# Optimization experiments

Measured on AMD Instinct MI355X. Metric: run time of the kernel, lower is better.

Reference implementation:

```python
import jax, jax.numpy as jnp
import numpy as np

N = 30000      # nodes
E = 480000     # edges
F = 128        # num_node_features (== C, required by LSTM-JK stacking of h_list incl. x)
C = 128        # graph_hidden_channels
K = 8          # kernel_size (num gaussians)
D = 2          # pseudo-coordinate dim
L = 4          # nlayers
H = (L * C) // 2   # PyG JK-LSTM hidden size = 256
NHID = 512
NOUT = 256
B = 1024       # number of graphs in batch
EPS = 1e-15


def setup_inputs() -> dict:
    key = jax.random.key(0)
    ks = jax.random.split(key, 24)
    s = 0.05
    inp = {}
    inp['x'] = jax.random.normal(ks[0], (N, F), jnp.float32)
    inp['edge_index'] = jax.random.randint(ks[1], (2, E), 0, N, dtype=jnp.int32)
    inp['edge_attr'] = jax.random.uniform(ks[2], (E, D), jnp.float32)
    inp['batch'] = jnp.sort(jax.random.randint(ks[3], (N,), 0, B, dtype=jnp.int32))
    # GMMConv params per layer (Cin == C for all layers since F == C)
    inp['g'] = jax.random.normal(ks[4], (L, F, K * C), jnp.float32) * s
    inp['root'] = jax.random.normal(ks[5], (L, F, C), jnp.float32) * s
    inp['bias'] = jnp.zeros((L, C), jnp.float32)
    inp['mu'] = jax.random.uniform(ks[6], (L, K, D), jnp.float32)
    inp['sigma'] = jax.random.uniform(ks[7], (L, K, D), jnp.float32) * 0.5 + 0.5
    inp['bn_gamma'] = jnp.ones((L, C), jnp.float32)
    inp['bn_beta'] = jnp.zeros((L, C), jnp.float32)
    # Bidirectional LSTM for JumpingKnowledge: dir 0 = fwd, dir 1 = bwd; gate order i,f,g,o
    inp['w_ih'] = jax.random.normal(ks[8], (2, 4 * H, C), jnp.float32) * s
    inp['w_hh'] = jax.random.normal(ks[9], (2, 4 * H, H), jnp.float32) * s
    inp['b_ih'] = jnp.zeros((2, 4 * H), jnp.float32)
    inp['b_hh'] = jnp.zeros((2, 4 * H), jnp.float32)
    inp['att_w'] = jax.random.normal(ks[10], (2 * H, 1), jnp.float32) * s
    inp['att_b'] = jnp.zeros((1,), jnp.float32)
    inp['p1_w'] = jax.random.normal(ks[11], (C, NHID), jnp.float32) * s
    inp['p1_b'] = jnp.zeros((NHID,), jnp.float32)
    inp['p2_w'] = jax.random.normal(ks[12], (NHID, NOUT), jnp.float32) * s
    inp['p2_b'] = jnp.zeros((NOUT,), jnp.float32)
    inp['ln_g'] = jnp.ones((NOUT,), jnp.float32)
    inp['ln_b'] = jnp.zeros((NOUT,), jnp.float32)
    return inp


def _lstm_dir(xs, w_ih, w_hh, b_ih, b_hh, reverse):
    # xs: [T, N, C] -> hidden states [T, N, H], aligned with input order
    def step(carry, xt):
        h, c = carry
        gates = xt @ w_ih.T + h @ w_hh.T + (b_ih + b_hh)
        i, f, g, o = jnp.split(gates, 4, axis=-1)
        c = jax.nn.sigmoid(f) * c + jax.nn.sigmoid(i) * jnp.tanh(g)
        h = jax.nn.sigmoid(o) * jnp.tanh(c)
        return (h, c), h
    h0 = jnp.zeros((xs.shape[1], w_hh.shape[1]), xs.dtype)
    _, hs = jax.lax.scan(step, (h0, h0), xs, reverse=reverse)
    return hs


def reference(x, edge_index, edge_attr, batch, g, root, bias, mu, sigma,
              bn_gamma, bn_beta, w_ih, w_hh, b_ih, b_hh, att_w, att_b,
              p1_w, p1_b, p2_w, p2_b, ln_g, ln_b):
    src, dst = edge_index[0], edge_index[1]
    deg = jnp.maximum(jax.ops.segment_sum(jnp.ones((E,), x.dtype), dst, num_segments=N), 1.0)[:, None]
    h = x
    h_list = [x]
    for i in range(L):
        # GMMConv: node-level transform then gaussian-weighted message passing (mean aggr)
        xg = (h @ g[i]).reshape(N, K, C)                     # [N, K, C]
        diff = edge_attr[:, None, :] - mu[i][None]           # [E, K, D]
        w = jnp.exp(jnp.sum(-0.5 * diff ** 2 / (EPS + sigma[i][None] ** 2), axis=-1))  # [E, K]
        msg = jnp.zeros((E, C), x.dtype)
        for k in range(K):                                   # small fixed K; avoids [E,K,C] gather
            msg = msg + w[:, k:k + 1] * xg[src, k, :]
        agg = jax.ops.segment_sum(msg, dst, num_segments=N) / deg
        h = agg + h @ root[i] + bias[i]
        # BatchNorm1d (training-mode batch statistics)
        mean = h.mean(0)
        var = h.var(0)
        h = (h - mean) / jnp.sqrt(var + 1e-5) * bn_gamma[i] + bn_beta[i]
        if i < L - 1:
            h = jax.nn.relu(h)
        # dropout is identity in eval mode
        h_list.append(h)
    # JumpingKnowledge, mode='lstm'
    xs = jnp.stack(h_list, axis=0)                           # [L+1, N, C]
    hf = _lstm_dir(xs, w_ih[0], w_hh[0], b_ih[0], b_hh[0], False)
    hb = _lstm_dir(xs, w_ih[1], w_hh[1], b_ih[1], b_hh[1], True)
    seq = jnp.concatenate([hf, hb], axis=-1)                 # [L+1, N, 2H]
    alpha = (seq @ att_w)[..., 0] + att_b[0]                 # [L+1, N]
    alpha = jax.nn.softmax(alpha, axis=0)
    node_rep = jnp.sum(alpha[..., None] * xs, axis=0)        # [N, C]
    # global_mean_pool
    cnt = jnp.maximum(jax.ops.segment_sum(jnp.ones((N,), x.dtype), batch, num_segments=B), 1.0)
    h_graph = jax.ops.segment_sum(node_rep, batch, num_segments=B) / cnt[:, None]
    z = jax.nn.relu(h_graph @ p1_w + p1_b)
    z = z @ p2_w + p2_b
    zm = z.mean(-1, keepdims=True)
    zv = z.var(-1, keepdims=True)
    return (z - zm) / jnp.sqrt(zv + 1e-5) * ln_g + ln_b
```

## Files before the change

### kernel.cpp

```cpp
#include <hip/hip_runtime.h>
#include <hip/hip_bf16.h>
#include <math.h>

#define N_    30000
#define E_    480000
#define C_    128
#define K_    8
#define L_    4
#define H_    256
#define NHID_ 512
#define NOUT_ 256
#define B_    1024
#define SCAN_B 30

typedef __attribute__((ext_vector_type(8))) short short8;
typedef __attribute__((ext_vector_type(4))) float floatx4;
typedef __hip_bfloat16 bf16;

static inline size_t align256(size_t x){ return (x + 255) & ~(size_t)255; }

__device__ __forceinline__ void gload_lds16(const void* g, void* l){
  __builtin_amdgcn_global_load_lds((const __attribute__((address_space(1))) void*)g,
                                   (__attribute__((address_space(3))) void*)l, 16, 0, 0);
}
__device__ __forceinline__ float bf2f(short s){
  union { unsigned u; float f; } x; x.u = ((unsigned)(unsigned short)s) << 16; return x.f;
}
__device__ __forceinline__ float sigm_f(float x){ return __builtin_amdgcn_rcpf(1.f + __expf(-x)); }
__device__ __forceinline__ float tanh_f(float x){ return 1.f - 2.f*__builtin_amdgcn_rcpf(1.f + __expf(2.f*x)); }

__global__ void hist_k(const int* __restrict__ dst, int* __restrict__ cnt){
  int e = blockIdx.x*256 + threadIdx.x;
  if (e < E_) atomicAdd(&cnt[dst[e]], 1);
}

__global__ void scan1_k(const int* __restrict__ cnt, int* __restrict__ rowptr, int* __restrict__ btot){
  __shared__ int sh[1024];
  int i = blockIdx.x*1024 + (int)threadIdx.x;
  int v = (i < N_) ? cnt[i] : 0;
  sh[threadIdx.x] = v;
  __syncthreads();
  for (int o = 1; o < 1024; o <<= 1){
    int t = (threadIdx.x >= (unsigned)o) ? sh[threadIdx.x - o] : 0;
    __syncthreads();
    sh[threadIdx.x] += t;
    __syncthreads();
  }
  if (i < N_) rowptr[i] = sh[threadIdx.x] - v;
  if (threadIdx.x == 1023) btot[blockIdx.x] = sh[1023];
}
__global__ void scan2_k(const int* __restrict__ btot, int* __restrict__ boff){
  if (threadIdx.x == 0){
    int s = 0;
    for (int b = 0; b < SCAN_B; b++){ boff[b] = s; s += btot[b]; }
    boff[SCAN_B] = s;
  }
}
__global__ void scan3_k(int* __restrict__ rowptr, const int* __restrict__ boff){
  int i = blockIdx.x*1024 + (int)threadIdx.x;
  if (i < N_) rowptr[i] += boff[blockIdx.x];
  if (i == N_-1) rowptr[N_] = boff[SCAN_B];
}

__global__ void degf_k(const int* __restrict__ cnt, float* __restrict__ degf){
  int n = blockIdx.x*256 + threadIdx.x;
  if (n < N_) degf[n] = fmaxf((float)cnt[n], 1.0f);
}

__global__ void scatter_k(const int* __restrict__ src, const int* __restrict__ dst,
                          const float* __restrict__ ea,
                          const int* __restrict__ rowptr, int* __restrict__ fill,
                          int* __restrict__ srcsort, float* __restrict__ easort){
  int e = blockIdx.x*256 + threadIdx.x;
  if (e >= E_) return;
  int d = dst[e];
  int pos = rowptr[d] + atomicAdd(&fill[d], 1);
  srcsort[pos] = src[e];
  ((float2*)easort)[pos] = ((const float2*)ea)[e];
}

__global__ void cast_k(const float* __restrict__ in, bf16* __restrict__ out, int n){
  int i = blockIdx.x*256 + threadIdx.x;
  if (i < n) out[i] = __float2bfloat16(in[i]);
}
__global__ void tcast_k(const float* __restrict__ in, bf16* __restrict__ out, int R, int Cc){
  const float* ip = in + (size_t)blockIdx.y*R*Cc;
  bf16* op = out + (size_t)blockIdx.y*R*Cc;
  int i = blockIdx.x*256 + threadIdx.x;
  if (i >= R*Cc) return;
  int c = i / R, r = i - c*R;
  op[i] = __float2bfloat16(ip[(size_t)r*Cc + c]);
}
__global__ void gtcast_k(const float* __restrict__ in, bf16* __restrict__ out){
  const float* ip = in + (size_t)blockIdx.y*C_*(K_*C_);
  bf16* op = out + (size_t)blockIdx.y*C_*(K_*C_);
  int i = blockIdx.x*256 + threadIdx.x;
  int co = i >> 10;
  int rem = i & 1023;
  int k = rem >> 7, c = rem & 127;
  op[i] = __float2bfloat16(ip[(size_t)c*(K_*C_) + k*C_ + co]);
}
__global__ void permcast_k(const float* __restrict__ in, bf16* __restrict__ out, int Kdim){
  const float* ip = in + (size_t)blockIdx.y*1024*Kdim;
  bf16* op = out + (size_t)blockIdx.y*1024*Kdim;
  int i = blockIdx.x*256 + threadIdx.x;
  if (i >= 1024*Kdim) return;
  int r = i / Kdim, k = i - r*Kdim;
  int gsel = r >> 8, jj = r & 255;
  int p = ((jj >> 5) << 7) + (((jj >> 4) & 1) << 6) + (gsel << 4) + (jj & 15);
  op[(size_t)p*Kdim + k] = __float2bfloat16(ip[i]);
}
__global__ void biassum_k(const float* __restrict__ bih, const float* __restrict__ bhh,
                          float* __restrict__ bs){
  int i = blockIdx.x*256 + threadIdx.x;
  if (i < 2048) bs[i] = bih[i] + bhh[i];
}

template<int OUTBF16, int STATS>
__global__ __launch_bounds__(256)
void gemm_bf16_k(const bf16* __restrict__ A1, const bf16* __restrict__ B1, int K1,
                 const bf16* __restrict__ A2, const bf16* __restrict__ B2, int K2,
                 const float* __restrict__ bias1, const float* __restrict__ bias2,
                 void* __restrict__ Cout, int M, int Nn, int relu,
                 float* __restrict__ stats)
{
  __shared__ short As[128*32];
  __shared__ short Bs[128*32];
  __shared__ float colstat[256];
  const int tid  = threadIdx.x;
  const int wave = tid >> 6, lane = tid & 63;
  const int m0 = blockIdx.y*128, n0 = blockIdx.x*128;
  const int wm = (wave >> 1)*64, wn = (wave & 1)*64;
  const int lrow = lane & 15, lk = lane >> 4;
  floatx4 acc[4][4] = {};
  if (STATS) colstat[tid] = 0.f;

  #pragma unroll
  for (int phase = 0; phase < 2; ++phase){
    const bf16* A = phase ? A2 : A1;
    const bf16* B = phase ? B2 : B1;
    const int   K = phase ? K2 : K1;
    if (A == nullptr) continue;
    for (int k0 = 0; k0 < K; k0 += 32){
      #pragma unroll
      for (int i = 0; i < 2; ++i){
        const int c    = i*256 + wave*64 + lane;
        const int row  = c >> 2;
        const int jsrc = (c & 3) ^ ((c >> 3) & 3);
        int ar = m0 + row; if (ar >= M) ar = M - 1;
        gload_lds16(A + (size_t)ar*K + k0 + jsrc*8,         As + (size_t)c*8);
        gload_lds16(B + (size_t)(n0 + row)*K + k0 + jsrc*8, Bs + (size_t)c*8);
      }
      __syncthreads();
      short8 af[4], bfr[4];
      #pragma unroll
      for (int t = 0; t < 4; ++t){
        const int ra = wm + t*16 + lrow;
        const int rb = wn + t*16 + lrow;
        af[t]  = *(const short8*)&As[(ra*4 + (lk ^ ((ra >> 1) & 3)))*8];
        bfr[t] = *(const short8*)&Bs[(rb*4 + (lk ^ ((rb >> 1) & 3)))*8];
      }
      #pragma unroll
      for (int mt = 0; mt < 4; ++mt)
        #pragma unroll
        for (int nt = 0; nt < 4; ++nt)
          acc[mt][nt] = __builtin_amdgcn_mfma_f32_16x16x32_bf16(af[mt], bfr[nt], acc[mt][nt], 0, 0, 0);
      __syncthreads();
    }
  }

  float* outf = (float*)Cout;
  bf16*  outb = (bf16*)Cout;
  #pragma unroll
  for (int nt = 0; nt < 4; ++nt){
    const int col = n0 + wn + nt*16 + lrow;
    float bv = bias1 ? bias1[col] : 0.f;
    if (bias2) bv += bias2[col];
    float s = 0.f, s2 = 0.f;
    #pragma unroll
    for (int mt = 0; mt < 4; ++mt){
      #pragma unroll
      for (int r = 0; r < 4; ++r){
        const int row = m0 + wm + mt*16 + lk*4 + r;
        if (row >= M) continue;
        float v = acc[mt][nt][r] + bv;
        if (relu) v = fmaxf(v, 0.f);
        if (OUTBF16) outb[(size_t)row*Nn + col] = __float2bfloat16(v);
        else         outf[(size_t)row*Nn + col] = v;
        if (STATS){ s += v; s2 += v*v; }
      }
    }
    if (STATS){
      s  += __shfl_down(s, 16);  s  += __shfl_down(s, 32);
      s2 += __shfl_down(s2, 16); s2 += __shfl_down(s2, 32);
      if (lane < 16){
        atomicAdd(&colstat[wn + nt*16 + lane], s);
        atomicAdd(&colstat[128 + wn + nt*16 + lane], s2);
      }
    }
  }
  if (STATS){
    __syncthreads();
    if (tid < 128){
      atomicAdd(&stats[tid],       colstat[tid]);
      atomicAdd(&stats[128 + tid], colstat[128 + tid]);
    }
  }
}

__global__ __launch_bounds__(256)
void lstm_step2_k(const bf16* __restrict__ A1f, const bf16* __restrict__ A1b,
                  const bf16* __restrict__ wihp, const bf16* __restrict__ whhp,
                  const bf16* __restrict__ hpf, const bf16* __restrict__ hpb,
                  const float* __restrict__ bsum,
                  bf16* __restrict__ hof, bf16* __restrict__ hob,
                  bf16* __restrict__ csf, bf16* __restrict__ csb,
                  const float* __restrict__ attw,
                  float* __restrict__ alf, float* __restrict__ alb,
                  int M)
{
  __shared__ short As[128*32];
  __shared__ short Bs[128*32];
  const int dir = blockIdx.z;
  const bf16* A1 = dir ? A1b : A1f;
  const bf16* A2 = dir ? hpb : hpf;
  const bf16* B1 = wihp + (size_t)dir*4*H_*C_;
  const bf16* B2 = whhp + (size_t)dir*4*H_*H_;
  bf16* hout = dir ? hob : hof;
  bf16* cst  = dir ? csb : csf;
  float* alpha = dir ? alb : alf;
  const float* bsd = bsum + (size_t)dir*4*H_;
  const float* awd = attw + (size_t)dir*H_;

  const int tid  = threadIdx.x;
  const int wave = tid >> 6, lane = tid & 63;
  const int m0 = blockIdx.y*128, n0 = blockIdx.x*128;
  const int wm = (wave >> 1)*64, wn = (wave & 1)*64;
  const int lrow = lane & 15, lk = lane >> 4;
  floatx4 acc[4][4] = {};

  #pragma unroll
  for (int phase = 0; phase < 2; ++phase){
    const bf16* A = phase ? A2 : A1;
    const bf16* B = phase ? B2 : B1;
    const int   K = phase ? H_ : C_;
    if (A == nullptr) continue;
    for (int k0 = 0; k0 < K; k0 += 32){
      #pragma unroll
      for (int i = 0; i < 2; ++i){
        const int c    = i*256 + wave*64 + lane;
        const int row  = c >> 2;
        const int jsrc = (c & 3) ^ ((c >> 3) & 3);
        int ar = m0 + row; if (ar >= M) ar = M - 1;
        gload_lds16(A + (size_t)ar*K + k0 + jsrc*8,         As + (size_t)c*8);
        gload_lds16(B + (size_t)(n0 + row)*K + k0 + jsrc*8, Bs + (size_t)c*8);
      }
      __syncthreads();
      short8 af[4], bfr[4];
      #pragma unroll
      for (int t = 0; t < 4; ++t){
        const int ra = wm + t*16 + lrow;
        const int rb = wn + t*16 + lrow;
        af[t]  = *(const short8*)&As[(ra*4 + (lk ^ ((ra >> 1) & 3)))*8];
        bfr[t] = *(const short8*)&Bs[(rb*4 + (lk ^ ((rb >> 1) & 3)))*8];
      }
      #pragma unroll
      for (int mt = 0; mt < 4; ++mt)
        #pragma unroll
        for (int nt = 0; nt < 4; ++nt)
          acc[mt][nt] = __builtin_amdgcn_mfma_f32_16x16x32_bf16(af[mt], bfr[nt], acc[mt][nt], 0, 0, 0);
      __syncthreads();
    }
  }

  const int j  = blockIdx.x*32 + (wave & 1)*16 + lrow;
  const float bi = bsd[0*H_ + j], bff = bsd[1*H_ + j];
  const float bg = bsd[2*H_ + j], bo  = bsd[3*H_ + j];
  const float aw = awd[j];
  #pragma unroll
  for (int mt = 0; mt < 4; ++mt){
    #pragma unroll
    for (int r = 0; r < 4; ++r){
      const int row = m0 + wm + mt*16 + lk*4 + r;
      const bool ok = row < M;
      const size_t idx = (size_t)row*H_ + j;
      float co = 0.f;
      if (A2 && ok) co = __bfloat162float(cst[idx]);
      float ig = sigm_f(acc[mt][0][r] + bi);
      float fg = sigm_f(acc[mt][1][r] + bff);
      float gt = tanh_f(acc[mt][2][r] + bg);
      float og = sigm_f(acc[mt][3][r] + bo);
      float cv = fg*co + ig*gt;
      float hv = og*tanh_f(cv);
      if (ok && hout){
        cst[idx]  = __float2bfloat16(cv);
        hout[idx] = __float2bfloat16(hv);
      }
      float att = ok ? hv*aw : 0.f;
      att += __shfl_xor(att, 1);
      att += __shfl_xor(att, 2);
      att += __shfl_xor(att, 4);
      att += __shfl_xor(att, 8);
      if (lrow == 0 && ok) atomicAdd(&alpha[row], att);
    }
  }
}

__global__ void compute_w_k(const float* __restrict__ easort, const float* __restrict__ mu,
                            const float* __restrict__ sigma, bf16* __restrict__ wsrt)
{
  int e = blockIdx.x*256 + threadIdx.x;
  if (e >= E_) return;
  float2 a = ((const float2*)easort)[e];
  short8 o;
  #pragma unroll
  for (int k = 0; k < 8; k++){
    float d0 = a.x - mu[2*k],  d1 = a.y - mu[2*k+1];
    float s0 = sigma[2*k],     s1 = sigma[2*k+1];
    float t = -0.5f*(d0*d0/(1e-15f + s0*s0) + d1*d1/(1e-15f + s1*s1));
    o[k] = __builtin_bit_cast(short, __float2bfloat16(expf(t)));
  }
  *(short8*)(wsrt + (size_t)e*8) = o;
}

__global__ __launch_bounds__(256)
void aggregate_t_k(const bf16* __restrict__ h, const bf16* __restrict__ wsrt,
                   const int* __restrict__ rowptr, const int* __restrict__ srcsort,
                   const float* __restrict__ degf, bf16* __restrict__ t)
{
  int node = blockIdx.x*4 + (threadIdx.x >> 6);
  int lane = threadIdx.x & 63;
  if (node >= N_) return;
  int p0 = rowptr[node], p1 = rowptr[node+1];
  float ax[8] = {}, ay[8] = {};
  for (int p = p0; p < p1; p++){
    int s = srcsort[p];
    short8 wv = *(const short8*)(wsrt + (size_t)p*8);
    float2 v = __bfloat1622float2(((const __hip_bfloat162*)(h + (size_t)s*C_))[lane]);
    #pragma unroll
    for (int k = 0; k < 8; k++){
      float wk = bf2f(wv[k]);
      ax[k] = fmaf(wk, v.x, ax[k]);
      ay[k] = fmaf(wk, v.y, ay[k]);
    }
  }
  float inv = 1.0f / degf[node];
  __hip_bfloat162* tp = (__hip_bfloat162*)(t + (size_t)node*(K_*C_));
  #pragma unroll
  for (int k = 0; k < 8; k++){
    __hip_bfloat162 o; o.x = __float2bfloat16(ax[k]*inv); o.y = __float2bfloat16(ay[k]*inv);
    tp[k*64 + lane] = o;
  }
}

__global__ void bn_apply_k(const float* __restrict__ hpre, const float* __restrict__ stats,
                           const float* __restrict__ gamma, const float* __restrict__ beta,
                           bf16* __restrict__ outp, int relu)
{
  int i = blockIdx.x*256 + threadIdx.x;
  if (i >= N_*C_) return;
  int c = i & 127;
  float mean = stats[c] * (1.0f/N_);
  float var  = stats[c+128] * (1.0f/N_) - mean*mean;
  float rstd = rsqrtf(var + 1e-5f);
  float v = (hpre[i] - mean)*rstd*gamma[c] + beta[c];
  if (relu) v = fmaxf(v, 0.f);
  outp[i] = __float2bfloat16(v);
}

__global__ void jk_pool_k(const float* __restrict__ x, const bf16* __restrict__ hlist,
                          const float* __restrict__ alpha, const int* __restrict__ batch,
                          float* __restrict__ hgraph, float* __restrict__ gcnt)
{
  int n = blockIdx.x, c = threadIdx.x;
  float a[5]; float mx = -1e30f;
  #pragma unroll
  for (int t = 0; t < 5; t++){ a[t] = alpha[(size_t)t*N_ + n]; mx = fmaxf(mx, a[t]); }
  float ssum = 0.f;
  #pragma unroll
  for (int t = 0; t < 5; t++){ a[t] = expf(a[t] - mx); ssum += a[t]; }
  float inv = 1.0f/ssum;
  float val = a[0]*inv*x[(size_t)n*C_ + c];
  #pragma unroll
  for (int t = 1; t < 5; t++)
    val = fmaf(a[t]*inv, __bfloat162float(hlist[((size_t)(t-1)*N_ + n)*C_ + c]), val);
  int bg = batch[n];
  atomicAdd(&hgraph[(size_t)bg*C_ + c], val);
  if (c == 0) atomicAdd(&gcnt[bg], 1.0f);
}

__global__ void pool_div_k(const float* __restrict__ hg, const float* __restrict__ gcnt,
                           bf16* __restrict__ hgb){
  int i = blockIdx.x*256 + threadIdx.x;
  if (i < B_*C_) hgb[i] = __float2bfloat16(hg[i] / fmaxf(gcnt[i >> 7], 1.0f));
}

__global__ __launch_bounds__(256)
void layernorm_k(float* __restrict__ z, const float* __restrict__ g, const float* __restrict__ b){
  int row = blockIdx.x, j = threadIdx.x;
  float v = z[(size_t)row*NOUT_ + j];
  float s = v, s2 = v*v;
  #pragma unroll
  for (int o = 32; o; o >>= 1){ s += __shfl_down(s, o); s2 += __shfl_down(s2, o); }
  __shared__ float sh[8];
  int w = j >> 6;
  if ((j & 63) == 0){ sh[w] = s; sh[4+w] = s2; }
  __syncthreads();
  float st  = sh[0] + sh[1] + sh[2] + sh[3];
  float st2 = sh[4] + sh[5] + sh[6] + sh[7];
  float mean = st * (1.0f/NOUT_);
  float var  = st2 * (1.0f/NOUT_) - mean*mean;
  float rstd = rsqrtf(var + 1e-5f);
  z[(size_t)row*NOUT_ + j] = (v - mean)*rstd*g[j] + b[j];
}

extern "C" void kernel_launch(void* const* d_in, const int* in_sizes, int n_in,
                              void* d_out, int out_size, void* d_ws, size_t ws_size,
                              hipStream_t stream)
{
  (void)in_sizes; (void)n_in; (void)out_size; (void)ws_size;
  const float* x     = (const float*)d_in[0];
  const int*   eidx  = (const int*)  d_in[1];
  const float* eattr = (const float*)d_in[2];
  const int*   batch = (const int*)  d_in[3];
  const float* g     = (const float*)d_in[4];
  const float* root  = (const float*)d_in[5];
  const float* bias  = (const float*)d_in[6];
  const float* mu    = (const float*)d_in[7];
  const float* sigma = (const float*)d_in[8];
  const float* bng   = (const float*)d_in[9];
  const float* bnb   = (const float*)d_in[10];
  const float* w_ih  = (const float*)d_in[11];
  const float* w_hh  = (const float*)d_in[12];
  const float* b_ih  = (const float*)d_in[13];
  const float* b_hh  = (const float*)d_in[14];
  const float* attw  = (const float*)d_in[15];
  const float* p1w   = (const float*)d_in[17];
  const float* p1b   = (const float*)d_in[18];
  const float* p2w   = (const float*)d_in[19];
  const float* p2b   = (const float*)d_in[20];
  const float* lng   = (const float*)d_in[21];
  const float* lnb   = (const float*)d_in[22];
  float* outp = (float*)d_out;

  const int* src = eidx;
  const int* dst = eidx + E_;

  size_t off = 0;
  char* wsb = (char*)d_ws;
  auto carve = [&](size_t bytes)->void*{ void* p = wsb + off; off = align256(off + bytes); return p; };
  bf16*  hlist  = (bf16*) carve((size_t)L_*N_*C_*2);
  void*  big    =         carve((size_t)N_*(K_*C_)*2);
  void*  uni    =         carve((size_t)6*N_*H_*2 + 256);
  bf16*  xb     = (bf16*) carve((size_t)N_*C_*2);
  float* alpha  = (float*)carve((size_t)(L_+1)*N_*4);
  float* hgraph = (float*)carve((size_t)B_*C_*4);
  bf16*  hgb    = (bf16*) carve((size_t)B_*C_*2);
  float* gcnt   = (float*)carve((size_t)B_*4);
  bf16*  z1b    = (bf16*) carve((size_t)B_*NHID_*2);
  float* bnstats= (float*)carve((size_t)L_*2*C_*4);
  float* degf   = (float*)carve((size_t)N_*4);
  int* cnt      = (int*)  carve((size_t)N_*4);
  int* rowptr   = (int*)  carve((size_t)(N_+1)*4);
  int* fill     = (int*)  carve((size_t)N_*4);
  int* srcsort  = (int*)  carve((size_t)E_*4);
  float* easort = (float*)carve((size_t)E_*2*4);
  int* btot     = (int*)  carve((size_t)(SCAN_B+1)*4);
  int* boff     = (int*)  carve((size_t)(SCAN_B+1)*4);
  bf16* gGT   = (bf16*)carve((size_t)L_*C_*(K_*C_)*2);
  bf16* rootT = (bf16*)carve((size_t)L_*C_*C_*2);
  bf16* wihp  = (bf16*)carve((size_t)2*4*H_*C_*2);
  bf16* whhp  = (bf16*)carve((size_t)2*4*H_*H_*2);
  float* bsum = (float*)carve((size_t)2*4*H_*4);
  bf16* p1T   = (bf16*)carve((size_t)NHID_*C_*2);
  bf16* p2T   = (bf16*)carve((size_t)NOUT_*NHID_*2);

  bf16*  wsrt   = (bf16*)uni;
  float* hpre   = (float*)((char*)uni + (size_t)E_*K_*2);
  bf16*  hAf    = (bf16*)uni;
  bf16*  hAb    = hAf + (size_t)N_*H_;
  bf16*  hBf    = hAb + (size_t)N_*H_;
  bf16*  hBb    = hBf + (size_t)N_*H_;
  bf16*  csf    = hBb + (size_t)N_*H_;
  bf16*  csb    = csf + (size_t)N_*H_;
  bf16*  tbuf   = (bf16*)big;

  hipMemsetAsync(cnt,     0, (size_t)N_*4, stream);
  hipMemsetAsync(fill,    0, (size_t)N_*4, stream);
  hipMemsetAsync(bnstats, 0, (size_t)L_*2*C_*4, stream);
  hipMemsetAsync(hgraph,  0, (size_t)B_*C_*4, stream);
  hipMemsetAsync(gcnt,    0, (size_t)B_*4, stream);
  hipMemsetAsync(alpha,   0, (size_t)(L_+1)*N_*4, stream);

  const dim3 blk(256);

  hist_k  <<<(E_+255)/256, 256, 0, stream>>>(dst, cnt);
  scan1_k <<<SCAN_B, 1024, 0, stream>>>(cnt, rowptr, btot);
  scan2_k <<<1, 64, 0, stream>>>(btot, boff);
  scan3_k <<<SCAN_B, 1024, 0, stream>>>(rowptr, boff);
  degf_k  <<<(N_+255)/256, 256, 0, stream>>>(cnt, degf);
  scatter_k<<<(E_+255)/256, 256, 0, stream>>>(src, dst, eattr, rowptr, fill, srcsort, easort);

  cast_k <<<(N_*C_+255)/256, blk, 0, stream>>>(x, xb, N_*C_);
  gtcast_k<<<dim3((C_*K_*C_)/256, L_), blk, 0, stream>>>(g, gGT);
  tcast_k<<<dim3((C_*C_+255)/256,   L_), blk, 0, stream>>>(root, rootT, C_,   C_);
  permcast_k<<<dim3((1024*C_+255)/256, 2), blk, 0, stream>>>(w_ih, wihp, C_);
  permcast_k<<<dim3((1024*H_+255)/256, 2), blk, 0, stream>>>(w_hh, whhp, H_);
  biassum_k<<<8, blk, 0, stream>>>(b_ih, b_hh, bsum);
  tcast_k<<<dim3((C_*NHID_+255)/256, 1), blk, 0, stream>>>(p1w, p1T, C_,    NHID_);
  tcast_k<<<dim3((NHID_*NOUT_+255)/256,1), blk, 0, stream>>>(p2w, p2T, NHID_, NOUT_);

  const int MB = (N_ + 127)/128;

  for (int l = 0; l < L_; l++){
    const bf16* hin = l ? (hlist + (size_t)(l-1)*N_*C_) : xb;
    compute_w_k<<<(E_+255)/256, blk, 0, stream>>>(easort, mu + (size_t)l*K_*2, sigma + (size_t)l*K_*2, wsrt);
    aggregate_t_k<<<N_/4, blk, 0, stream>>>(hin, wsrt, rowptr, srcsort, degf, tbuf);
    gemm_bf16_k<0,1><<<dim3(C_/128, MB), blk, 0, stream>>>(
        tbuf, gGT + (size_t)l*C_*K_*C_, K_*C_, hin, rootT + (size_t)l*C_*C_, C_,
        bias + (size_t)l*C_, nullptr, hpre, N_, C_, 0, bnstats + l*2*C_);
    bn_apply_k<<<(N_*C_+255)/256, blk, 0, stream>>>(hpre, bnstats + l*2*C_, bng + (size_t)l*C_, bnb + (size_t)l*C_,
                                                    hlist + (size_t)l*N_*C_, (l < L_-1) ? 1 : 0);
  }

  {
    const bf16 *hpf = nullptr, *hpb = nullptr;
    for (int s = 0; s < 5; s++){
      int tf = s, tb = 4 - s;
      const bf16* xtf = tf ? (hlist + (size_t)(tf-1)*N_*C_) : xb;
      const bf16* xtb = tb ? (hlist + (size_t)(tb-1)*N_*C_) : xb;
      bf16* hof = (s == 4) ? nullptr : ((s & 1) ? hBf : hAf);
      bf16* hob = (s == 4) ? nullptr : ((s & 1) ? hBb : hAb);
      lstm_step2_k<<<dim3(8, MB, 2), blk, 0, stream>>>(
          xtf, xtb, wihp, whhp, hpf, hpb, bsum, hof, hob, csf, csb,
          attw, alpha + (size_t)tf*N_, alpha + (size_t)tb*N_, N_);
      hpf = hof; hpb = hob;
    }
  }

  jk_pool_k<<<N_, 128, 0, stream>>>(x, hlist, alpha, batch, hgraph, gcnt);
  pool_div_k<<<(B_*C_+255)/256, blk, 0, stream>>>(hgraph, gcnt, hgb);

  gemm_bf16_k<1,0><<<dim3(NHID_/128, B_/128), blk, 0, stream>>>(
      hgb, p1T, C_, nullptr, nullptr, 0, p1b, nullptr, z1b, B_, NHID_, 1, nullptr);
  gemm_bf16_k<0,0><<<dim3(NOUT_/128, B_/128), blk, 0, stream>>>(
      z1b, p2T, NHID_, nullptr, nullptr, 0, p2b, nullptr, outp, B_, NOUT_, 0, nullptr);
  layernorm_k<<<B_, 256, 0, stream>>>(outp, lng, lnb);
}
```

Baseline: 1.233 ms.

## Split GMM GEMM along K across two blocks and widen LSTM step tiles

The per-layer GMM GEMM (K=1024+128) ran with only ~235 blocks, so it is now split along K into two z-slices, each writing a separate fp32 partial. BN statistics move into a separate reduction kernel that sums the two partials, and BN apply adds them as well. The LSTM step kernel changes to 512-thread blocks with 256-wide N tiles, which halves the grid and reuses each loaded A tile across more output columns. The cost is an extra fp32 N×C buffer to write and read, plus one more kernel launch per layer.

```diff
diff --git a/kernel.cpp b/kernel.cpp
--- a/kernel.cpp
+++ b/kernel.cpp
@@ -116,24 +116,21 @@
   if (i < 2048) bs[i] = bih[i] + bhh[i];
 }
 
-template<int OUTBF16, int STATS>
+template<int OUTBF16>
 __global__ __launch_bounds__(256)
 void gemm_bf16_k(const bf16* __restrict__ A1, const bf16* __restrict__ B1, int K1,
                  const bf16* __restrict__ A2, const bf16* __restrict__ B2, int K2,
-                 const float* __restrict__ bias1, const float* __restrict__ bias2,
-                 void* __restrict__ Cout, int M, int Nn, int relu,
-                 float* __restrict__ stats)
+                 const float* __restrict__ bias1,
+                 void* __restrict__ Cout, int M, int Nn, int relu)
 {
   __shared__ short As[128*32];
   __shared__ short Bs[128*32];
-  __shared__ float colstat[256];
   const int tid  = threadIdx.x;
   const int wave = tid >> 6, lane = tid & 63;
   const int m0 = blockIdx.y*128, n0 = blockIdx.x*128;
   const int wm = (wave >> 1)*64, wn = (wave & 1)*64;
   const int lrow = lane & 15, lk = lane >> 4;
   floatx4 acc[4][4] = {};
-  if (STATS) colstat[tid] = 0.f;
 
   #pragma unroll
   for (int phase = 0; phase < 2; ++phase){
@@ -175,8 +172,6 @@
   for (int nt = 0; nt < 4; ++nt){
     const int col = n0 + wn + nt*16 + lrow;
     float bv = bias1 ? bias1[col] : 0.f;
-    if (bias2) bv += bias2[col];
-    float s = 0.f, s2 = 0.f;
     #pragma unroll
     for (int mt = 0; mt < 4; ++mt){
       #pragma unroll
@@ -187,28 +182,84 @@
         if (relu) v = fmaxf(v, 0.f);
         if (OUTBF16) outb[(size_t)row*Nn + col] = __float2bfloat16(v);
         else         outf[(size_t)row*Nn + col] = v;
-        if (STATS){ s += v; s2 += v*v; }
-      }
-    }
-    if (STATS){
-      s  += __shfl_down(s, 16);  s  += __shfl_down(s, 32);
-      s2 += __shfl_down(s2, 16); s2 += __shfl_down(s2, 32);
-      if (lane < 16){
-        atomicAdd(&colstat[wn + nt*16 + lane], s);
-        atomicAdd(&colstat[128 + wn + nt*16 + lane], s2);
-      }
-    }
-  }
-  if (STATS){
-    __syncthreads();
-    if (tid < 128){
-      atomicAdd(&stats[tid],       colstat[tid]);
-      atomicAdd(&stats[128 + tid], colstat[128 + tid]);
+      }
     }
   }
 }
 
 __global__ __launch_bounds__(256)
+void gmm_split_k(const bf16* __restrict__ tbuf, const bf16* __restrict__ gGTl,
+                 const bf16* __restrict__ hin, const bf16* __restrict__ rootTl,
+                 const float* __restrict__ bias,
+                 float* __restrict__ outA, float* __restrict__ outB, int M)
+{
+  __shared__ short As[128*32];
+  __shared__ short Bs[128*32];
+  const int z = blockIdx.z;
+  const int tid  = threadIdx.x;
+  const int wave = tid >> 6, lane = tid & 63;
+  const int m0 = blockIdx.x*128;
+  const int wm = (wave >> 1)*64, wn = (wave & 1)*64;
+  const int lrow = lane & 15, lk = lane >> 4;
+  floatx4 acc[4][4] = {};
+
+  const int k1off = z ? 576 : 0;
+  const int k1len = z ? 448 : 576;
+
+  #pragma unroll
+  for (int phase = 0; phase < 2; ++phase){
+    if (phase == 1 && z == 0) break;
+    const bf16* A   = phase ? hin    : tbuf;
+    const bf16* B   = phase ? rootTl : gGTl;
+    const int   ld  = phase ? C_     : (K_*C_);
+    const int   kof = phase ? 0      : k1off;
+    const int   Kl  = phase ? C_     : k1len;
+    for (int k0 = 0; k0 < Kl; k0 += 32){
+      #pragma unroll
+      for (int i = 0; i < 2; ++i){
+        const int c    = i*256 + wave*64 + lane;
+        const int row  = c >> 2;
+        const int jsrc = (c & 3) ^ ((c >> 3) & 3);
+        int ar = m0 + row; if (ar >= M) ar = M - 1;
+        gload_lds16(A + (size_t)ar*ld + kof + k0 + jsrc*8, As + (size_t)c*8);
+        gload_lds16(B + (size_t)row*ld + kof + k0 + jsrc*8, Bs + (size_t)c*8);
+      }
+      __syncthreads();
+      short8 af[4], bfr[4];
+      #pragma unroll
+      for (int t = 0; t < 4; ++t){
+        const int ra = wm + t*16 + lrow;
+        const int rb = wn + t*16 + lrow;
+        af[t]  = *(const short8*)&As[(ra*4 + (lk ^ ((ra >> 1) & 3)))*8];
+        bfr[t] = *(const short8*)&Bs[(rb*4 + (lk ^ ((rb >> 1) & 3)))*8];
+      }
+      #pragma unroll
+      for (int mt = 0; mt < 4; ++mt)
+        #pragma unroll
+        for (int nt = 0; nt < 4; ++nt)
+          acc[mt][nt] = __builtin_amdgcn_mfma_f32_16x16x32_bf16(af[mt], bfr[nt], acc[mt][nt], 0, 0, 0);
+      __syncthreads();
+    }
+  }
+
+  float* out = z ? outB : outA;
+  #pragma unroll
+  for (int nt = 0; nt < 4; ++nt){
+    const int col = wn + nt*16 + lrow;
+    const float bv = z ? 0.f : bias[col];
+    #pragma unroll
+    for (int mt = 0; mt < 4; ++mt){
+      #pragma unroll
+      for (int r = 0; r < 4; ++r){
+        const int row = m0 + wm + mt*16 + lk*4 + r;
+        if (row >= M) continue;
+        out[(size_t)row*C_ + col] = acc[mt][nt][r] + bv;
+      }
+    }
+  }
+}
+
+__global__ __launch_bounds__(512)
 void lstm_step2_k(const bf16* __restrict__ A1f, const bf16* __restrict__ A1b,
                   const bf16* __restrict__ wihp, const bf16* __restrict__ whhp,
                   const bf16* __restrict__ hpf, const bf16* __restrict__ hpb,
@@ -220,7 +271,7 @@
                   int M)
 {
   __shared__ short As[128*32];
-  __shared__ short Bs[128*32];
+  __shared__ short Bs[256*32];
   const int dir = blockIdx.z;
   const bf16* A1 = dir ? A1b : A1f;
   const bf16* A2 = dir ? hpb : hpf;
@@ -234,8 +285,8 @@
 
   const int tid  = threadIdx.x;
   const int wave = tid >> 6, lane = tid & 63;
-  const int m0 = blockIdx.y*128, n0 = blockIdx.x*128;
-  const int wm = (wave >> 1)*64, wn = (wave & 1)*64;
+  const int m0 = blockIdx.y*128, n0 = blockIdx.x*256;
+  const int wm = (wave >> 2)*64, wn = (wave & 3)*64;
   const int lrow = lane & 15, lk = lane >> 4;
   floatx4 acc[4][4] = {};
 
@@ -247,13 +298,16 @@
     if (A == nullptr) continue;
     for (int k0 = 0; k0 < K; k0 += 32){
       #pragma unroll
-      for (int i = 0; i < 2; ++i){
-        const int c    = i*256 + wave*64 + lane;
-        const int row  = c >> 2;
-        const int jsrc = (c & 3) ^ ((c >> 3) & 3);
-        int ar = m0 + row; if (ar >= M) ar = M - 1;
-        gload_lds16(A + (size_t)ar*K + k0 + jsrc*8,         As + (size_t)c*8);
-        gload_lds16(B + (size_t)(n0 + row)*K + k0 + jsrc*8, Bs + (size_t)c*8);
+      for (int i = 0; i < 3; ++i){
+        const int t = i*512 + wave*64 + lane;
+        if (t < 512){
+          const int c = t, row = c >> 2, jsrc = (c & 3) ^ ((c >> 3) & 3);
+          int ar = m0 + row; if (ar >= M) ar = M - 1;
+          gload_lds16(A + (size_t)ar*K + k0 + jsrc*8, As + (size_t)c*8);
+        } else {
+          const int c = t - 512, row = c >> 2, jsrc = (c & 3) ^ ((c >> 3) & 3);
+          gload_lds16(B + (size_t)(n0 + row)*K + k0 + jsrc*8, Bs + (size_t)c*8);
+        }
       }
       __syncthreads();
       short8 af[4], bfr[4];
@@ -273,7 +327,8 @@
     }
   }
 
-  const int j  = blockIdx.x*32 + (wave & 1)*16 + lrow;
+  const int q = (n0 + wn) >> 6;
+  const int j = (q >> 1)*32 + (q & 1)*16 + lrow;
   const float bi = bsd[0*H_ + j], bff = bsd[1*H_ + j];
   const float bg = bsd[2*H_ + j], bo  = bsd[3*H_ + j];
   const float aw = awd[j];
@@ -353,9 +408,26 @@
   }
 }
 
-__global__ void bn_apply_k(const float* __restrict__ hpre, const float* __restrict__ stats,
-                           const float* __restrict__ gamma, const float* __restrict__ beta,
-                           bf16* __restrict__ outp, int relu)
+__global__ __launch_bounds__(256)
+void gmm_stats2_k(const float* __restrict__ hA, const float* __restrict__ hB,
+                  float* __restrict__ stats)
+{
+  int c = threadIdx.x & 127;
+  int sub = threadIdx.x >> 7;
+  float s = 0.f, s2 = 0.f;
+  for (int r = blockIdx.x*2 + sub; r < N_; r += gridDim.x*2){
+    size_t i = (size_t)r*C_ + c;
+    float v = hA[i] + hB[i];
+    s += v; s2 += v*v;
+  }
+  atomicAdd(&stats[c], s);
+  atomicAdd(&stats[c+128], s2);
+}
+
+__global__ void bn_apply2_k(const float* __restrict__ hA, const float* __restrict__ hB,
+                            const float* __restrict__ stats,
+                            const float* __restrict__ gamma, const float* __restrict__ beta,
+                            bf16* __restrict__ outp, int relu)
 {
   int i = blockIdx.x*256 + threadIdx.x;
   if (i >= N_*C_) return;
@@ -363,7 +435,7 @@
   float mean = stats[c] * (1.0f/N_);
   float var  = stats[c+128] * (1.0f/N_) - mean*mean;
   float rstd = rsqrtf(var + 1e-5f);
-  float v = (hpre[i] - mean)*rstd*gamma[c] + beta[c];
+  float v = ((hA[i] + hB[i]) - mean)*rstd*gamma[c] + beta[c];
   if (relu) v = fmaxf(v, 0.f);
   outp[i] = __float2bfloat16(v);
 }
@@ -476,7 +548,8 @@
   bf16* p2T   = (bf16*)carve((size_t)NOUT_*NHID_*2);
 
   bf16*  wsrt   = (bf16*)uni;
-  float* hpre   = (float*)((char*)uni + (size_t)E_*K_*2);
+  float* hpreA  = (float*)((char*)uni + (size_t)E_*K_*2);
+  float* hpreB  = hpreA + (size_t)N_*C_;
   bf16*  hAf    = (bf16*)uni;
   bf16*  hAb    = hAf + (size_t)N_*H_;
   bf16*  hBf    = hAb + (size_t)N_*H_;
@@ -516,11 +589,12 @@
     const bf16* hin = l ? (hlist + (size_t)(l-1)*N_*C_) : xb;
     compute_w_k<<<(E_+255)/256, blk, 0, stream>>>(easort, mu + (size_t)l*K_*2, sigma + (size_t)l*K_*2, wsrt);
     aggregate_t_k<<<N_/4, blk, 0, stream>>>(hin, wsrt, rowptr, srcsort, degf, tbuf);
-    gemm_bf16_k<0,1><<<dim3(C_/128, MB), blk, 0, stream>>>(
-        tbuf, gGT + (size_t)l*C_*K_*C_, K_*C_, hin, rootT + (size_t)l*C_*C_, C_,
-        bias + (size_t)l*C_, nullptr, hpre, N_, C_, 0, bnstats + l*2*C_);
-    bn_apply_k<<<(N_*C_+255)/256, blk, 0, stream>>>(hpre, bnstats + l*2*C_, bng + (size_t)l*C_, bnb + (size_t)l*C_,
-                                                    hlist + (size_t)l*N_*C_, (l < L_-1) ? 1 : 0);
+    gmm_split_k<<<dim3(MB, 1, 2), blk, 0, stream>>>(
+        tbuf, gGT + (size_t)l*C_*K_*C_, hin, rootT + (size_t)l*C_*C_,
+        bias + (size_t)l*C_, hpreA, hpreB, N_);
+    gmm_stats2_k<<<120, blk, 0, stream>>>(hpreA, hpreB, bnstats + l*2*C_);
+    bn_apply2_k<<<(N_*C_+255)/256, blk, 0, stream>>>(hpreA, hpreB, bnstats + l*2*C_,
+        bng + (size_t)l*C_, bnb + (size_t)l*C_, hlist + (size_t)l*N_*C_, (l < L_-1) ? 1 : 0);
   }
 
   {
@@ -531,7 +605,7 @@
       const bf16* xtb = tb ? (hlist + (size_t)(tb-1)*N_*C_) : xb;
       bf16* hof = (s == 4) ? nullptr : ((s & 1) ? hBf : hAf);
       bf16* hob = (s == 4) ? nullptr : ((s & 1) ? hBb : hAb);
-      lstm_step2_k<<<dim3(8, MB, 2), blk, 0, stream>>>(
+      lstm_step2_k<<<dim3(4, MB, 2), 512, 0, stream>>>(
           xtf, xtb, wihp, whhp, hpf, hpb, bsum, hof, hob, csf, csb,
           attw, alpha + (size_t)tf*N_, alpha + (size_t)tb*N_, N_);
       hpf = hof; hpb = hob;
@@ -541,9 +615,9 @@
   jk_pool_k<<<N_, 128, 0, stream>>>(x, hlist, alpha, batch, hgraph, gcnt);
   pool_div_k<<<(B_*C_+255)/256, blk, 0, stream>>>(hgraph, gcnt, hgb);
 
-  gemm_bf16_k<1,0><<<dim3(NHID_/128, B_/128), blk, 0, stream>>>(
-      hgb, p1T, C_, nullptr, nullptr, 0, p1b, nullptr, z1b, B_, NHID_, 1, nullptr);
-  gemm_bf16_k<0,0><<<dim3(NOUT_/128, B_/128), blk, 0, stream>>>(
-      z1b, p2T, NHID_, nullptr, nullptr, 0, p2b, nullptr, outp, B_, NOUT_, 0, nullptr);
+  gemm_bf16_k<1><<<dim3(NHID_/128, B_/128), blk, 0, stream>>>(
+      hgb, p1T, C_, nullptr, nullptr, 0, p1b, z1b, B_, NHID_, 1);
+  gemm_bf16_k<0><<<dim3(NOUT_/128, B_/128), blk, 0, stream>>>(
+      z1b, p2T, NHID_, nullptr, nullptr, 0, p2b, outp, B_, NOUT_, 0);
   layernorm_k<<<B_, 256, 0, stream>>>(outp, lng, lnb);
 }
```

Measured after the change: 1.539 ms. 24.8% more time.
